# Performance work log

Hardware: AMD Instinct MI355X
Metric: run time of the kernel (lower is better)

Reference implementation:

```python
import jax, jax.numpy as jnp
import numpy as np

N, E, DIN, DOUT, H = 50000, 800000, 256, 128, 8
DH = DOUT // H  # per-head dim = 16


def setup_inputs() -> dict:
    key = jax.random.key(0)
    k1, k2, k3, k4, k5 = jax.random.split(key, 5)
    x = jax.random.normal(k1, (N, DIN), dtype=jnp.float32)
    edge_index = jax.random.randint(k2, (2, E), 0, N)
    W_trans = jax.random.normal(k3, (DOUT, DIN), dtype=jnp.float32) / np.sqrt(DIN).astype(np.float32)
    W_att = jax.random.normal(k4, (1, 2 * DH), dtype=jnp.float32) / np.sqrt(2 * DH).astype(np.float32)
    b_att = jax.random.normal(k5, (1,), dtype=jnp.float32) * 0.01
    return {"x": x, "W_trans": W_trans, "W_att": W_att, "b_att": b_att, "edge_index": edge_index}


def reference(x, W_trans, W_att, b_att, edge_index):
    n = x.shape[0]
    # append self-loops (as in the torch module)
    loops = jnp.arange(n, dtype=edge_index.dtype)
    ei = jnp.concatenate([edge_index, jnp.stack([loops, loops])], axis=1)  # [2, E+N]
    src, dst = ei[0], ei[1]

    # linear transform, split heads: [n, H, DH]
    h = (x @ W_trans.T).reshape(n, H, DH)
    h_i = h[src]  # [Etot, H, DH]
    h_j = h[dst]  # [Etot, H, DH]

    # per-edge attention score: concat -> linear -> leaky_relu(0.2)
    s = jnp.concatenate([h_i, h_j], axis=-1) @ W_att.T + b_att  # [Etot, H, 1]
    s = jnp.where(s >= 0, s, 0.2 * s)

    # softmax(dim=0)*exp_sum/scatter_add(exp) == exp(s)/segment_sum(exp(s)) per dst node
    e = jnp.exp(s)
    denom = jax.ops.segment_sum(e, dst, num_segments=n)  # [n, H, 1]
    att = e / denom[dst]

    out = jax.ops.segment_sum(h_i * att, dst, num_segments=n)  # [n, H, DH]
    return out.reshape(n, DOUT)  # head_fusion='cat'
```

## Files before the change

### kernel.cpp

```cpp
#include <hip/hip_runtime.h>


constexpr int DIN  = 256;
constexpr int DOUT = 128;
constexpr int H    = 8;
constexpr int CAP  = 5120;
constexpr int CHUNK = 4096;

typedef __attribute__((ext_vector_type(8))) short bf16x8;
typedef __attribute__((ext_vector_type(4))) float f32x4;

__device__ __forceinline__ float lrelu(float s) { return s >= 0.0f ? s : 0.2f * s; }

__device__ __forceinline__ unsigned short f2bf(float f) {
  unsigned u = __float_as_uint(f);
  u += 0x7FFF + ((u >> 16) & 1);
  return (unsigned short)(u >> 16);
}
__device__ __forceinline__ float bflo(unsigned u) { return __uint_as_float(u << 16); }
__device__ __forceinline__ float bfhi(unsigned u) { return __uint_as_float(u & 0xFFFF0000u); }

__device__ __forceinline__ int wave_incl_scan(int v, int lane) {
#pragma unroll
  for (int d = 1; d < 64; d <<= 1) {
    int t = __shfl_up(v, d, 64);
    if (lane >= d) v += t;
  }
  return v;
}

__global__ void conv_w(const float* __restrict__ W, unsigned short* __restrict__ Wbf,
                       int n, int* __restrict__ bcount, int nb) {
  int i = blockIdx.x * blockDim.x + threadIdx.x;
  if (i < n) Wbf[i] = f2bf(W[i]);
  if (blockIdx.x == 0 && threadIdx.x < nb) bcount[threadIdx.x] = 0;
}

__global__ __launch_bounds__(256) void bp_gemm(const float* __restrict__ x,
                                               const unsigned short* __restrict__ Wbf,
                                               unsigned short* __restrict__ hbf, int N,
                                               const int* __restrict__ ei,
                                               int* __restrict__ bcount,
                                               unsigned* __restrict__ pair_buf,
                                               int E, int nb, int bp_blocks) {
  __shared__ int hist[256];
  __shared__ int gbase[256];
  if ((int)blockIdx.x < bp_blocks) {
    int c0 = blockIdx.x * CHUNK;
    hist[threadIdx.x] = 0;
    __syncthreads();
    int dcache[16];
#pragma unroll
    for (int q = 0; q < 16; ++q) {
      int e = c0 + q * 256 + threadIdx.x;
      dcache[q] = (e < E) ? ei[E + e] : -1;
      if (dcache[q] >= 0) atomicAdd(&hist[dcache[q] >> 8], 1);
    }
    __syncthreads();
    if (threadIdx.x < nb) {
      int c = hist[threadIdx.x];
      gbase[threadIdx.x] = c ? atomicAdd(&bcount[threadIdx.x], c) : 0;
    }
    __syncthreads();
    hist[threadIdx.x] = 0;
    __syncthreads();
#pragma unroll
    for (int q = 0; q < 16; ++q) {
      int e = c0 + q * 256 + threadIdx.x;
      if (dcache[q] >= 0) {
        int s = ei[e];
        int bk = dcache[q] >> 8;
        int r = atomicAdd(&hist[bk], 1);
        pair_buf[bk * CAP + gbase[bk] + r] = ((unsigned)s << 8) | (unsigned)(dcache[q] & 255);
      }
    }
    return;
  }
  int wid = (blockIdx.x - bp_blocks) * 4 + (threadIdx.x >> 6);
  int m0 = wid * 16;
  if (m0 >= N) return;
  int lane = threadIdx.x & 63;
  int mr = lane & 15;
  int kg = lane >> 4;
  int rr = m0 + mr;
  if (rr >= N) rr = N - 1;
  const float* xrow = x + (size_t)rr * DIN + kg * 8;

  f32x4 acc[8];
#pragma unroll
  for (int t = 0; t < 8; ++t) acc[t] = (f32x4){0.f, 0.f, 0.f, 0.f};

#pragma unroll
  for (int ks = 0; ks < 8; ++ks) {
    float4 alo = *(const float4*)(xrow + ks * 32);
    float4 ahi = *(const float4*)(xrow + ks * 32 + 4);
    bf16x8 a;
    a[0] = (short)f2bf(alo.x); a[1] = (short)f2bf(alo.y);
    a[2] = (short)f2bf(alo.z); a[3] = (short)f2bf(alo.w);
    a[4] = (short)f2bf(ahi.x); a[5] = (short)f2bf(ahi.y);
    a[6] = (short)f2bf(ahi.z); a[7] = (short)f2bf(ahi.w);
#pragma unroll
    for (int t = 0; t < 8; ++t) {
      bf16x8 b = *(const bf16x8*)(Wbf + ((size_t)(t * 16 + mr) * DIN + ks * 32 + kg * 8));
      acc[t] = __builtin_amdgcn_mfma_f32_16x16x32_bf16(a, b, acc[t], 0, 0, 0);
    }
  }
#pragma unroll
  for (int t = 0; t < 8; ++t) {
#pragma unroll
    for (int r = 0; r < 4; ++r) {
      int row = m0 + kg * 4 + r;
      if (row < N) hbf[(size_t)row * DOUT + t * 16 + mr] = f2bf(acc[t][r]);
    }
  }
}

__global__ __launch_bounds__(256) void fs_ns(const unsigned* __restrict__ pair_buf,
                                             const int* __restrict__ bcount,
                                             int* __restrict__ offsets,
                                             unsigned short* __restrict__ src_sorted,
                                             const unsigned short* __restrict__ hbf,
                                             const float* __restrict__ Wa,
                                             float* __restrict__ a_src,
                                             float* __restrict__ a_dst,
                                             int N, int E, int nb) {
  __shared__ int cnt[256];
  __shared__ int cur[256];
  __shared__ int redS[256];
  __shared__ int wsumS[4];
  const int t = threadIdx.x;
  if ((int)blockIdx.x >= nb) {
    int idx = ((int)blockIdx.x - nb) * 256 + t;
    if (idx >= N * H) return;
    int v = idx >> 3, hh = idx & 7;
    const unsigned short* hp = hbf + (size_t)v * DOUT + hh * 16;
    uint4 p0 = *(const uint4*)hp;
    uint4 p1 = *(const uint4*)(hp + 8);
    float hv[16];
    hv[0] = bflo(p0.x); hv[1] = bfhi(p0.x); hv[2] = bflo(p0.y); hv[3] = bfhi(p0.y);
    hv[4] = bflo(p0.z); hv[5] = bfhi(p0.z); hv[6] = bflo(p0.w); hv[7] = bfhi(p0.w);
    hv[8] = bflo(p1.x); hv[9] = bfhi(p1.x); hv[10] = bflo(p1.y); hv[11] = bfhi(p1.y);
    hv[12] = bflo(p1.z); hv[13] = bfhi(p1.z); hv[14] = bflo(p1.w); hv[15] = bfhi(p1.w);
    float s1 = 0.f, s2 = 0.f;
#pragma unroll
    for (int d = 0; d < 16; ++d) {
      s1 += hv[d] * Wa[d];
      s2 += hv[d] * Wa[16 + d];
    }
    a_src[idx] = s1;
    a_dst[idx] = s2;
    return;
  }
  const int B = blockIdx.x;
  const int node0 = B * 256;
  const int v = node0 + t;
  const int valid = (v < N);
  cnt[t] = valid ? 1 : 0;
  __syncthreads();
  const int cntE = bcount[B];
  const unsigned* reg = pair_buf + B * CAP;
  for (int i = t; i < cntE; i += 256)
    atomicAdd(&cnt[reg[i] & 255], 1);
  redS[t] = (t < B) ? bcount[t] : 0;
  __syncthreads();
  for (int s = 128; s > 0; s >>= 1) {
    if (t < s) redS[t] += redS[t + s];
    __syncthreads();
  }
  const int csr_base = redS[0] + node0;
  int val = cnt[t];
  int lane = t & 63, wv = t >> 6;
  int inc = wave_incl_scan(val, lane);
  if (lane == 63) wsumS[wv] = inc;
  __syncthreads();
  int base = 0;
  for (int q = 0; q < wv; ++q) base += wsumS[q];
  int ex = base + inc - val;
  cur[t] = ex + 1;
  if (valid) {
    offsets[v] = csr_base + ex;
    src_sorted[csr_base + ex] = (unsigned short)v;
  }
  if (B == 0 && t == 0) offsets[N] = E + N;
  __syncthreads();
  for (int i = t; i < cntE; i += 256) {
    unsigned p = reg[i];
    int k = atomicAdd(&cur[p & 255], 1);
    src_sorted[csr_base + k] = (unsigned short)(p >> 8);
  }
}

__global__ __launch_bounds__(256) void aggregate(const unsigned short* __restrict__ hbf,
                                                 const float* __restrict__ a_src,
                                                 const float* __restrict__ a_dst,
                                                 const float* __restrict__ b_att,
                                                 const int* __restrict__ offsets,
                                                 const unsigned short* __restrict__ src_sorted,
                                                 float* __restrict__ out, int N) {
  int wid = blockIdx.x * 4 + (threadIdx.x >> 6);
  if (wid >= N) return;
  int lane = threadIdx.x & 63;
  int g = lane >> 4, sl = lane & 15;
  int head = sl >> 1;
  float adv = a_dst[wid * H + head] + b_att[0];
  int beg = offsets[wid], end = offsets[wid + 1];
  float a0 = 0, a1 = 0, a2 = 0, a3 = 0, a4 = 0, a5 = 0, a6 = 0, a7 = 0, den = 0;
  for (int j0 = beg; j0 < end; j0 += 8) {
    int ja = j0 + g, jb = j0 + 4 + g;
    bool va = ja < end, vb = jb < end;
    int sa = src_sorted[va ? ja : beg];
    int sb = src_sorted[vb ? jb : beg];
    float asa = a_src[sa * H + head];
    float asb = a_src[sb * H + head];
    uint4 ua = *(const uint4*)(hbf + sa * DOUT + sl * 8);
    uint4 ub = *(const uint4*)(hbf + sb * DOUT + sl * 8);
    float ea = va ? __expf(lrelu(asa + adv)) : 0.f;
    float eb = vb ? __expf(lrelu(asb + adv)) : 0.f;
    den += ea + eb;
    a0 += ea * bflo(ua.x) + eb * bflo(ub.x);
    a1 += ea * bfhi(ua.x) + eb * bfhi(ub.x);
    a2 += ea * bflo(ua.y) + eb * bflo(ub.y);
    a3 += ea * bfhi(ua.y) + eb * bfhi(ub.y);
    a4 += ea * bflo(ua.z) + eb * bflo(ub.z);
    a5 += ea * bfhi(ua.z) + eb * bfhi(ub.z);
    a6 += ea * bflo(ua.w) + eb * bflo(ub.w);
    a7 += ea * bfhi(ua.w) + eb * bfhi(ub.w);
  }
  den += __shfl_xor(den, 16, 64); den += __shfl_xor(den, 32, 64);
  a0 += __shfl_xor(a0, 16, 64); a0 += __shfl_xor(a0, 32, 64);
  a1 += __shfl_xor(a1, 16, 64); a1 += __shfl_xor(a1, 32, 64);
  a2 += __shfl_xor(a2, 16, 64); a2 += __shfl_xor(a2, 32, 64);
  a3 += __shfl_xor(a3, 16, 64); a3 += __shfl_xor(a3, 32, 64);
  a4 += __shfl_xor(a4, 16, 64); a4 += __shfl_xor(a4, 32, 64);
  a5 += __shfl_xor(a5, 16, 64); a5 += __shfl_xor(a5, 32, 64);
  a6 += __shfl_xor(a6, 16, 64); a6 += __shfl_xor(a6, 32, 64);
  a7 += __shfl_xor(a7, 16, 64); a7 += __shfl_xor(a7, 32, 64);
  float inv = 1.0f / den;
  if (g == 0) {
    float4 o = make_float4(a0 * inv, a1 * inv, a2 * inv, a3 * inv);
    *(float4*)&out[wid * DOUT + sl * 8] = o;
  } else if (g == 1) {
    float4 o = make_float4(a4 * inv, a5 * inv, a6 * inv, a7 * inv);
    *(float4*)&out[wid * DOUT + sl * 8 + 4] = o;
  }
}

extern "C" void kernel_launch(void* const* d_in, const int* in_sizes, int n_in,
                              void* d_out, int out_size, void* d_ws, size_t ws_size,
                              hipStream_t stream) {
  const float* x     = (const float*)d_in[0];
  const float* W     = (const float*)d_in[1];
  const float* Wa    = (const float*)d_in[2];
  const float* b_att = (const float*)d_in[3];
  const int*   ei    = (const int*)d_in[4];
  const int N  = in_sizes[0] / DIN;
  const int E  = in_sizes[4] / 2;
  const int NB = (N + 255) / 256;
  float* out = (float*)d_out;

  char* p = (char*)d_ws;
  auto take = [&p](size_t bytes) {
    uintptr_t u = ((uintptr_t)p + 15) & ~(uintptr_t)15;
    p = (char*)(u + bytes);
    return (void*)u;
  };
  unsigned short* hbf = (unsigned short*)take((size_t)N * DOUT * 2);
  unsigned short* Wbf = (unsigned short*)take((size_t)DOUT * DIN * 2);
  float* a_src        = (float*)take((size_t)N * H * 4);
  float* a_dst        = (float*)take((size_t)N * H * 4);
  int* bcount         = (int*)take((size_t)NB * 4);
  unsigned* pair_buf  = (unsigned*)take((size_t)NB * CAP * 4);
  int* offsets        = (int*)take((size_t)(N + 1) * 4);
  unsigned short* src_sorted = (unsigned short*)take((size_t)(E + N + 16) * 2);

  dim3 b256(256);
  const int bp_blocks   = (E + CHUNK - 1) / CHUNK;
  const int gemm_blocks = ((N + 15) / 16 + 3) / 4;
  const int ns_blocks   = (N * H + 255) / 256;

  conv_w<<<dim3((DOUT * DIN + 255) / 256), b256, 0, stream>>>(W, Wbf, DOUT * DIN, bcount, NB);
  bp_gemm<<<dim3(bp_blocks + gemm_blocks), b256, 0, stream>>>(
      x, Wbf, hbf, N, ei, bcount, pair_buf, E, NB, bp_blocks);
  fs_ns<<<dim3(NB + ns_blocks), b256, 0, stream>>>(
      pair_buf, bcount, offsets, src_sorted, hbf, Wa, a_src, a_dst, N, E, NB);
  aggregate<<<dim3((N + 3) / 4), b256, 0, stream>>>(hbf, a_src, a_dst, b_att, offsets,
                                                    src_sorted, out, N);
}
```

Measured before the change: 185.0 us.

## Split CSR fill into quarter-bucket blocks with finer per-64-node counts

The bucket pass now records per-64-node counts (bcount4) in addition to the per-256-node bucket cursor. The CSR fill launches four blocks per bucket, each handling 64 destination nodes, instead of one block per bucket. This spreads the fill over more blocks and shrinks each block's scan. The cost is that every quarter block rereads the whole bucket's pair buffer and filters it, so pair-buffer traffic rises fourfold and global atomics on the counts increase.

```diff
diff --git a/kernel.cpp b/kernel.cpp
--- a/kernel.cpp
+++ b/kernel.cpp
@@ -30,47 +30,53 @@
 }
 
 __global__ void conv_w(const float* __restrict__ W, unsigned short* __restrict__ Wbf,
-                       int n, int* __restrict__ bcount, int nb) {
+                       int n, int* __restrict__ bcount4, int* __restrict__ bcursor,
+                       int nq, int nb) {
   int i = blockIdx.x * blockDim.x + threadIdx.x;
   if (i < n) Wbf[i] = f2bf(W[i]);
-  if (blockIdx.x == 0 && threadIdx.x < nb) bcount[threadIdx.x] = 0;
+  if (i < nq) bcount4[i] = 0;
+  if (i < nb) bcursor[i] = 0;
 }
 
 __global__ __launch_bounds__(256) void bp_gemm(const float* __restrict__ x,
                                                const unsigned short* __restrict__ Wbf,
                                                unsigned short* __restrict__ hbf, int N,
                                                const int* __restrict__ ei,
-                                               int* __restrict__ bcount,
+                                               int* __restrict__ bcount4,
+                                               int* __restrict__ bcursor,
                                                unsigned* __restrict__ pair_buf,
                                                int E, int nb, int bp_blocks) {
-  __shared__ int hist[256];
-  __shared__ int gbase[256];
+  __shared__ int hist[784];
+  __shared__ int gbase[196];
+  __shared__ int bcur[196];
   if ((int)blockIdx.x < bp_blocks) {
+    const int t = threadIdx.x;
     int c0 = blockIdx.x * CHUNK;
-    hist[threadIdx.x] = 0;
+    for (int i = t; i < 784; i += 256) hist[i] = 0;
     __syncthreads();
     int dcache[16];
 #pragma unroll
     for (int q = 0; q < 16; ++q) {
-      int e = c0 + q * 256 + threadIdx.x;
+      int e = c0 + q * 256 + t;
       dcache[q] = (e < E) ? ei[E + e] : -1;
-      if (dcache[q] >= 0) atomicAdd(&hist[dcache[q] >> 8], 1);
+      if (dcache[q] >= 0) atomicAdd(&hist[dcache[q] >> 6], 1);
     }
     __syncthreads();
-    if (threadIdx.x < nb) {
-      int c = hist[threadIdx.x];
-      gbase[threadIdx.x] = c ? atomicAdd(&bcount[threadIdx.x], c) : 0;
-    }
+    if (t < nb) {
+      int c = hist[t * 4] + hist[t * 4 + 1] + hist[t * 4 + 2] + hist[t * 4 + 3];
+      gbase[t] = c ? atomicAdd(&bcursor[t], c) : 0;
+      bcur[t] = 0;
+    }
+    for (int i = t; i < 784; i += 256)
+      if (hist[i]) atomicAdd(&bcount4[i], hist[i]);
     __syncthreads();
-    hist[threadIdx.x] = 0;
-    __syncthreads();
 #pragma unroll
     for (int q = 0; q < 16; ++q) {
-      int e = c0 + q * 256 + threadIdx.x;
+      int e = c0 + q * 256 + t;
       if (dcache[q] >= 0) {
         int s = ei[e];
         int bk = dcache[q] >> 8;
-        int r = atomicAdd(&hist[bk], 1);
+        int r = atomicAdd(&bcur[bk], 1);
         pair_buf[bk * CAP + gbase[bk] + r] = ((unsigned)s << 8) | (unsigned)(dcache[q] & 255);
       }
     }
@@ -116,21 +122,20 @@
 }
 
 __global__ __launch_bounds__(256) void fs_ns(const unsigned* __restrict__ pair_buf,
-                                             const int* __restrict__ bcount,
+                                             const int* __restrict__ bcount4,
                                              int* __restrict__ offsets,
                                              unsigned short* __restrict__ src_sorted,
                                              const unsigned short* __restrict__ hbf,
                                              const float* __restrict__ Wa,
                                              float* __restrict__ a_src,
                                              float* __restrict__ a_dst,
-                                             int N, int E, int nb) {
-  __shared__ int cnt[256];
-  __shared__ int cur[256];
+                                             int N, int E, int fs_blocks) {
+  __shared__ int cnt[64];
+  __shared__ int cur[64];
   __shared__ int redS[256];
-  __shared__ int wsumS[4];
   const int t = threadIdx.x;
-  if ((int)blockIdx.x >= nb) {
-    int idx = ((int)blockIdx.x - nb) * 256 + t;
+  if ((int)blockIdx.x >= fs_blocks) {
+    int idx = ((int)blockIdx.x - fs_blocks) * 256 + t;
     if (idx >= N * H) return;
     int v = idx >> 3, hh = idx & 7;
     const unsigned short* hp = hbf + (size_t)v * DOUT + hh * 16;
@@ -151,42 +156,49 @@
     a_dst[idx] = s2;
     return;
   }
-  const int B = blockIdx.x;
-  const int node0 = B * 256;
-  const int v = node0 + t;
-  const int valid = (v < N);
-  cnt[t] = valid ? 1 : 0;
-  __syncthreads();
-  const int cntE = bcount[B];
-  const unsigned* reg = pair_buf + B * CAP;
-  for (int i = t; i < cntE; i += 256)
-    atomicAdd(&cnt[reg[i] & 255], 1);
-  redS[t] = (t < B) ? bcount[t] : 0;
+  const int qidx = blockIdx.x;
+  const int B = qidx >> 2, q = qidx & 3;
+  const int node0 = qidx * 64;
+  int acc = 0;
+  for (int j = t; j < qidx; j += 256) acc += bcount4[j];
+  redS[t] = acc;
   __syncthreads();
   for (int s = 128; s > 0; s >>= 1) {
     if (t < s) redS[t] += redS[t + s];
     __syncthreads();
   }
   const int csr_base = redS[0] + node0;
-  int val = cnt[t];
-  int lane = t & 63, wv = t >> 6;
-  int inc = wave_incl_scan(val, lane);
-  if (lane == 63) wsumS[wv] = inc;
+  const int cntE = bcount4[B * 4] + bcount4[B * 4 + 1] +
+                   bcount4[B * 4 + 2] + bcount4[B * 4 + 3];
+  if (t < 64) cnt[t] = (node0 + t < N) ? 1 : 0;
   __syncthreads();
-  int base = 0;
-  for (int q = 0; q < wv; ++q) base += wsumS[q];
-  int ex = base + inc - val;
-  cur[t] = ex + 1;
-  if (valid) {
-    offsets[v] = csr_base + ex;
-    src_sorted[csr_base + ex] = (unsigned short)v;
-  }
-  if (B == 0 && t == 0) offsets[N] = E + N;
+  const unsigned* reg = pair_buf + B * CAP;
+  for (int i = t; i < cntE; i += 256) {
+    unsigned p = reg[i];
+    int dl = p & 255;
+    if ((dl >> 6) == q) atomicAdd(&cnt[dl & 63], 1);
+  }
+  __syncthreads();
+  if (t < 64) {
+    int val = cnt[t];
+    int inc = wave_incl_scan(val, t);
+    int ex = inc - val;
+    cur[t] = ex + 1;
+    int v = node0 + t;
+    if (v < N) {
+      offsets[v] = csr_base + ex;
+      src_sorted[csr_base + ex] = (unsigned short)v;
+    }
+  }
+  if (qidx == 0 && t == 0) offsets[N] = E + N;
   __syncthreads();
   for (int i = t; i < cntE; i += 256) {
     unsigned p = reg[i];
-    int k = atomicAdd(&cur[p & 255], 1);
-    src_sorted[csr_base + k] = (unsigned short)(p >> 8);
+    int dl = p & 255;
+    if ((dl >> 6) == q) {
+      int k = atomicAdd(&cur[dl & 63], 1);
+      src_sorted[csr_base + k] = (unsigned short)(p >> 8);
+    }
   }
 }
 
@@ -256,6 +268,7 @@
   const int N  = in_sizes[0] / DIN;
   const int E  = in_sizes[4] / 2;
   const int NB = (N + 255) / 256;
+  const int NQ = NB * 4;
   float* out = (float*)d_out;
 
   char* p = (char*)d_ws;
@@ -268,7 +281,8 @@
   unsigned short* Wbf = (unsigned short*)take((size_t)DOUT * DIN * 2);
   float* a_src        = (float*)take((size_t)N * H * 4);
   float* a_dst        = (float*)take((size_t)N * H * 4);
-  int* bcount         = (int*)take((size_t)NB * 4);
+  int* bcount4        = (int*)take((size_t)NQ * 4);
+  int* bcursor        = (int*)take((size_t)NB * 4);
   unsigned* pair_buf  = (unsigned*)take((size_t)NB * CAP * 4);
   int* offsets        = (int*)take((size_t)(N + 1) * 4);
   unsigned short* src_sorted = (unsigned short*)take((size_t)(E + N + 16) * 2);
@@ -278,11 +292,12 @@
   const int gemm_blocks = ((N + 15) / 16 + 3) / 4;
   const int ns_blocks   = (N * H + 255) / 256;
 
-  conv_w<<<dim3((DOUT * DIN + 255) / 256), b256, 0, stream>>>(W, Wbf, DOUT * DIN, bcount, NB);
+  conv_w<<<dim3((DOUT * DIN + 255) / 256), b256, 0, stream>>>(
+      W, Wbf, DOUT * DIN, bcount4, bcursor, NQ, NB);
   bp_gemm<<<dim3(bp_blocks + gemm_blocks), b256, 0, stream>>>(
-      x, Wbf, hbf, N, ei, bcount, pair_buf, E, NB, bp_blocks);
-  fs_ns<<<dim3(NB + ns_blocks), b256, 0, stream>>>(
-      pair_buf, bcount, offsets, src_sorted, hbf, Wa, a_src, a_dst, N, E, NB);
+      x, Wbf, hbf, N, ei, bcount4, bcursor, pair_buf, E, NB, bp_blocks);
+  fs_ns<<<dim3(NQ + ns_blocks), b256, 0, stream>>>(
+      pair_buf, bcount4, offsets, src_sorted, hbf, Wa, a_src, a_dst, N, E, NQ);
   aggregate<<<dim3((N + 3) / 4), b256, 0, stream>>>(hbf, a_src, a_dst, b_att, offsets,
                                                     src_sorted, out, N);
 }
```

Result: no change. 187.9 us (+1.5%).
